# Kernel tuning notes

Measured on AMD Instinct MI355X. Metric: run time of the kernel, lower is better.

Reference implementation:

```python
import jax, jax.numpy as jnp
import numpy as np

N = 1024   # codeword length (variable nodes)
M_CN = 512 # check nodes
DV = 3     # variable-node degree
DC = 6     # check-node degree
E = N * DV # edges = 3072
B = 128    # batch of codewords
CLIP = 0.999999


def _build_masks():
    rng = np.random.default_rng(0)
    vn = np.repeat(np.arange(N), DV)                    # [E] variable node of each edge
    cn = rng.permutation(np.repeat(np.arange(M_CN), DC))  # [E] check node of each edge
    off = ~np.eye(E, dtype=bool)
    vn2cn = ((cn[:, None] == cn[None, :]) & off).astype(np.float32)  # [E,E] same check, excl self
    cn2vn = ((vn[:, None] == vn[None, :]) & off).astype(np.float32)  # [E,E] same vn, excl self
    onehot = (vn[:, None] == np.arange(N)[None, :]).astype(np.float32)  # [E,N]
    first = np.clip(vn2cn @ onehot, 0.0, 1.0)           # [E,N] vns in same check, excl own edge
    out_mask = onehot.T.copy()                          # [N,E]
    bias_mat = onehot.T.copy()                          # [N,E] routes LLR[v] to its edges
    return first, cn2vn, vn2cn, out_mask, bias_mat


def setup_inputs() -> dict:
    key = jax.random.key(0)
    x = jax.random.normal(key, (B, N), dtype=jnp.float32) * 2.0  # channel LLRs
    first, cn2vn, vn2cn, out_mask, bias_mat = _build_masks()
    return {
        "x": x,
        "first_mask": jnp.asarray(first),
        "cn2vn_mask": jnp.asarray(cn2vn),
        "vn2cn_mask": jnp.asarray(vn2cn),
        "out_mask": jnp.asarray(out_mask),
        "bias_mat": jnp.asarray(bias_mat),
    }


def _cn_update(x, mask):
    # Faithful to CnUpdateLayer: out[:,i] = prod_j of (x[:,j]*mask[i,j]) over nonzero
    # masked entries (masked-off or exactly-zero entries treated as 1), and 0 if no
    # nonzero masked entry. Computed fused in log/sign domain via matmuls instead of
    # the original per-column Python loop.
    nz = (x != 0.0)
    logabs = jnp.where(nz, jnp.log(jnp.abs(jnp.where(nz, x, 1.0))), 0.0)  # [B,I]
    neg = ((x < 0.0) & nz).astype(x.dtype)
    s = logabs @ mask.T                          # [B,O] sum log|x_j| over masked j
    negcnt = neg @ mask.T                        # [B,O] number of negative factors
    cnt = nz.astype(x.dtype) @ mask.T            # [B,O] number of nonzero factors
    sign = 1.0 - 2.0 * (negcnt % 2.0)
    return jnp.where(cnt > 0.0, sign * jnp.exp(s), 0.0)


def reference(x, first_mask, cn2vn_mask, vn2cn_mask, out_mask, bias_mat):
    llr = x  # Channel_LLR; bias_scaling_vectors are identity matrices (no-ops)
    bias = llr @ bias_mat  # [B,E], reused each iteration

    def cn_to_llr(h):
        return 2.0 * jnp.arctanh(jnp.clip(h, -CLIP, CLIP))

    h = jnp.tanh(0.5 * x)
    h = cn_to_llr(_cn_update(h, first_mask))          # fc0
    out1 = jax.nn.sigmoid(h @ out_mask.T + llr)

    h = jnp.tanh(0.5 * (h @ cn2vn_mask.T + bias))     # fc1
    h = cn_to_llr(_cn_update(h, vn2cn_mask))          # fc2
    out2 = jax.nn.sigmoid(h @ out_mask.T + llr)

    h = jnp.tanh(0.5 * (h @ cn2vn_mask.T + bias))     # fc3
    h = cn_to_llr(_cn_update(h, vn2cn_mask))          # fc4
    out3 = jax.nn.sigmoid(h @ out_mask.T + llr)

    h = jnp.tanh(0.5 * (h @ cn2vn_mask.T + bias))     # fc5
    h = cn_to_llr(_cn_update(h, vn2cn_mask))          # fc6
    out4 = jax.nn.sigmoid(h @ out_mask.T + llr)

    h = jnp.tanh(0.5 * (h @ cn2vn_mask.T + bias))     # fc7
    h = cn_to_llr(_cn_update(h, vn2cn_mask))          # fc8
    out5 = jax.nn.sigmoid(h @ out_mask.T + llr)       # fc9 (out_mask) + identity-scaled LLR

    return (out5, out4, out3, out2, out1)
```

## Files before the change

### kernel.cpp

```cpp
#include <hip/hip_runtime.h>
#include <math.h>

namespace {
constexpr int kN = 1024;
constexpr int kE = 3072;
constexpr int kB = 128;
constexpr float kClip = 0.999999f;
}

#define RCP(x) __builtin_amdgcn_rcpf(x)

__global__ __launch_bounds__(256) void extract_partners_kernel(
    const uint4* __restrict__ mask, unsigned long long* __restrict__ part) {
  __shared__ int slots[4][8];
  const int wave = threadIdx.x >> 6, lane = threadIdx.x & 63;
  const int row = blockIdx.x * 4 + wave;
  const uint4* rp = mask + (size_t)row * (kE / 4);
  const int it0 = (row + 1) >> 8;

  uint4 vals[12];
#pragma unroll
  for (int it = 0; it < 12; ++it)
    if (it >= it0) vals[it] = rp[it * 64 + lane];

  const unsigned long long lt = (1ULL << lane) - 1ULL;
  int cnt = 0;
#pragma unroll
  for (int it = 0; it < 12; ++it) {
    if (it < it0) continue;
    uint4 v = vals[it];
    const int idx = it * 256 + lane * 4;
    const bool b0 = (v.x != 0u) & (idx + 0 > row);
    const bool b1 = (v.y != 0u) & (idx + 1 > row);
    const bool b2 = (v.z != 0u) & (idx + 2 > row);
    const bool b3 = (v.w != 0u) & (idx + 3 > row);
    unsigned long long m0 = __ballot(b0);
    unsigned long long m1 = __ballot(b1);
    unsigned long long m2 = __ballot(b2);
    unsigned long long m3 = __ballot(b3);
    int before = cnt + __popcll(m0 & lt) + __popcll(m1 & lt) +
                 __popcll(m2 & lt) + __popcll(m3 & lt);
    int own = 0;
    if (b0) slots[wave][min(before + own, 7)] = idx + 0;
    own += (int)((m0 >> lane) & 1ULL);
    if (b1) slots[wave][min(before + own, 7)] = idx + 1;
    own += (int)((m1 >> lane) & 1ULL);
    if (b2) slots[wave][min(before + own, 7)] = idx + 2;
    own += (int)((m2 >> lane) & 1ULL);
    if (b3) slots[wave][min(before + own, 7)] = idx + 3;
    cnt += __popcll(m0) + __popcll(m1) + __popcll(m2) + __popcll(m3);
  }
  __syncthreads();
  if (cnt == 5 && lane < 6) {
    int g[6];
    g[0] = row;
#pragma unroll
    for (int i = 0; i < 5; ++i) g[i + 1] = slots[wave][i];
    unsigned long long pk = 0;
    int sh = 0;
#pragma unroll
    for (int i = 0; i < 6; ++i)
      if (i != lane) {
        pk |= (unsigned long long)(g[i] & 0xFFF) << sh;
        sh += 12;
      }
    part[g[lane]] = pk;
  }
}

__global__ __launch_bounds__(1024) void bp_kernel(
    const float* __restrict__ x, const unsigned long long* __restrict__ part,
    float* __restrict__ out) {
  __shared__ float tm[kE];
  __shared__ float rm[kE];
  const int b = blockIdx.x;
  const int tid = threadIdx.x;

  const unsigned long long pk0 = part[tid];
  const unsigned long long pk1 = part[tid + 1024];
  const unsigned long long pk2 = part[tid + 2048];
  const int i00 = (int)(pk0 & 0xFFF), i01 = (int)((pk0 >> 12) & 0xFFF),
            i02 = (int)((pk0 >> 24) & 0xFFF), i03 = (int)((pk0 >> 36) & 0xFFF),
            i04 = (int)((pk0 >> 48) & 0xFFF);
  const int i10 = (int)(pk1 & 0xFFF), i11 = (int)((pk1 >> 12) & 0xFFF),
            i12 = (int)((pk1 >> 24) & 0xFFF), i13 = (int)((pk1 >> 36) & 0xFFF),
            i14 = (int)((pk1 >> 48) & 0xFFF);
  const int i20 = (int)(pk2 & 0xFFF), i21 = (int)((pk2 >> 12) & 0xFFF),
            i22 = (int)((pk2 >> 24) & 0xFFF), i23 = (int)((pk2 >> 36) & 0xFFF),
            i24 = (int)((pk2 >> 48) & 0xFFF);

  const float l = x[(size_t)b * kN + tid];
  const float E = __expf(l);
  tm[tid] = (E - 1.0f) * RCP(E + 1.0f);
  __syncthreads();

  {
    const int ii[3][5] = {{i00, i01, i02, i03, i04},
                          {i10, i11, i12, i13, i14},
                          {i20, i21, i22, i23, i24}};
#pragma unroll
    for (int i = 0; i < 3; ++i) {
      const int q0 = ii[i][0] / 3, q1 = ii[i][1] / 3, q2 = ii[i][2] / 3,
                q3 = ii[i][3] / 3, q4 = ii[i][4] / 3;
      float prod = tm[q0];
      float f1 = tm[q1], f2 = tm[q2], f3 = tm[q3], f4 = tm[q4];
      prod *= (q1 == q0) ? 1.0f : f1;
      prod *= (q2 == q0 || q2 == q1) ? 1.0f : f2;
      prod *= (q3 == q0 || q3 == q1 || q3 == q2) ? 1.0f : f3;
      prod *= (q4 == q0 || q4 == q1 || q4 == q2 || q4 == q3) ? 1.0f : f4;
      const float y = fminf(fmaxf(prod, -kClip), kClip);
      rm[tid + i * 1024] = (1.0f + y) * RCP(1.0f - y);
    }
  }
  __syncthreads();

  float* ob = out + (size_t)b * kN + tid;
#pragma unroll
  for (int k = 1; k <= 4; ++k) {
    const float r0 = rm[3 * tid], r1 = rm[3 * tid + 1], r2 = rm[3 * tid + 2];
    const float P = E * r0 * r1 * r2;
    ob[(size_t)(5 - k) * kB * kN] = P * RCP(1.0f + P);
    const float p0 = E * r1 * r2, p1 = E * r0 * r2, p2 = E * r0 * r1;
    tm[3 * tid]     = (p0 - 1.0f) * RCP(p0 + 1.0f);
    tm[3 * tid + 1] = (p1 - 1.0f) * RCP(p1 + 1.0f);
    tm[3 * tid + 2] = (p2 - 1.0f) * RCP(p2 + 1.0f);
    __syncthreads();
    {
      float y0 = tm[i00] * tm[i01] * tm[i02] * tm[i03] * tm[i04];
      float y = fminf(fmaxf(y0, -kClip), kClip);
      rm[tid] = (1.0f + y) * RCP(1.0f - y);
      y0 = tm[i10] * tm[i11] * tm[i12] * tm[i13] * tm[i14];
      y = fminf(fmaxf(y0, -kClip), kClip);
      rm[tid + 1024] = (1.0f + y) * RCP(1.0f - y);
      y0 = tm[i20] * tm[i21] * tm[i22] * tm[i23] * tm[i24];
      y = fminf(fmaxf(y0, -kClip), kClip);
      rm[tid + 2048] = (1.0f + y) * RCP(1.0f - y);
    }
    __syncthreads();
  }
  const float r0 = rm[3 * tid], r1 = rm[3 * tid + 1], r2 = rm[3 * tid + 2];
  const float P = E * r0 * r1 * r2;
  ob[0] = P * RCP(1.0f + P);
}

extern "C" void kernel_launch(void* const* d_in, const int* in_sizes, int n_in,
                              void* d_out, int out_size, void* d_ws, size_t ws_size,
                              hipStream_t stream) {
  const float* x = (const float*)d_in[0];
  const float* vn2cn = (const float*)d_in[3];
  unsigned long long* part = (unsigned long long*)d_ws;
  float* out = (float*)d_out;

  hipLaunchKernelGGL(extract_partners_kernel, dim3(kE / 4), dim3(256), 0, stream,
                     (const uint4*)vn2cn, part);
  hipLaunchKernelGGL(bp_kernel, dim3(kB), dim3(1024), 0, stream, x, part, out);
}
```

Baseline: 18.90 us.

## Remap edges to threads so check results stay in registers, double-buffer shared messages

Each thread now owns the three edges of its own variable node for check-node updates, so check results stay in registers and the rm shared array plus its barrier go away. Shared messages are double-buffered so each iteration needs only one __syncthreads. The ratio products are rewritten as numerator/denominator pairs to drop some reciprocals. The partner loads become strided (part[3*tid+i]), which may reduce coalescing, and the ratio form may change rounding slightly.

```diff
diff --git a/kernel.cpp b/kernel.cpp
--- a/kernel.cpp
+++ b/kernel.cpp
@@ -71,76 +71,86 @@
 __global__ __launch_bounds__(1024) void bp_kernel(
     const float* __restrict__ x, const unsigned long long* __restrict__ part,
     float* __restrict__ out) {
-  __shared__ float tm[kE];
-  __shared__ float rm[kE];
+  __shared__ float tmV[kN];
+  __shared__ float tmE[2][kE];
   const int b = blockIdx.x;
   const int tid = threadIdx.x;
 
-  const unsigned long long pk0 = part[tid];
-  const unsigned long long pk1 = part[tid + 1024];
-  const unsigned long long pk2 = part[tid + 2048];
-  const int i00 = (int)(pk0 & 0xFFF), i01 = (int)((pk0 >> 12) & 0xFFF),
-            i02 = (int)((pk0 >> 24) & 0xFFF), i03 = (int)((pk0 >> 36) & 0xFFF),
-            i04 = (int)((pk0 >> 48) & 0xFFF);
-  const int i10 = (int)(pk1 & 0xFFF), i11 = (int)((pk1 >> 12) & 0xFFF),
-            i12 = (int)((pk1 >> 24) & 0xFFF), i13 = (int)((pk1 >> 36) & 0xFFF),
-            i14 = (int)((pk1 >> 48) & 0xFFF);
-  const int i20 = (int)(pk2 & 0xFFF), i21 = (int)((pk2 >> 12) & 0xFFF),
-            i22 = (int)((pk2 >> 24) & 0xFFF), i23 = (int)((pk2 >> 36) & 0xFFF),
-            i24 = (int)((pk2 >> 48) & 0xFFF);
+  int idx[3][5];
+#pragma unroll
+  for (int i = 0; i < 3; ++i) {
+    const unsigned long long pk = part[3 * tid + i];
+#pragma unroll
+    for (int j = 0; j < 5; ++j) idx[i][j] = (int)((pk >> (12 * j)) & 0xFFF);
+  }
 
   const float l = x[(size_t)b * kN + tid];
   const float E = __expf(l);
-  tm[tid] = (E - 1.0f) * RCP(E + 1.0f);
+  tmV[tid] = (E - 1.0f) * RCP(E + 1.0f);
   __syncthreads();
 
-  {
-    const int ii[3][5] = {{i00, i01, i02, i03, i04},
-                          {i10, i11, i12, i13, i14},
-                          {i20, i21, i22, i23, i24}};
+  float y[3];
 #pragma unroll
-    for (int i = 0; i < 3; ++i) {
-      const int q0 = ii[i][0] / 3, q1 = ii[i][1] / 3, q2 = ii[i][2] / 3,
-                q3 = ii[i][3] / 3, q4 = ii[i][4] / 3;
-      float prod = tm[q0];
-      float f1 = tm[q1], f2 = tm[q2], f3 = tm[q3], f4 = tm[q4];
-      prod *= (q1 == q0) ? 1.0f : f1;
-      prod *= (q2 == q0 || q2 == q1) ? 1.0f : f2;
-      prod *= (q3 == q0 || q3 == q1 || q3 == q2) ? 1.0f : f3;
-      prod *= (q4 == q0 || q4 == q1 || q4 == q2 || q4 == q3) ? 1.0f : f4;
-      const float y = fminf(fmaxf(prod, -kClip), kClip);
-      rm[tid + i * 1024] = (1.0f + y) * RCP(1.0f - y);
-    }
+  for (int i = 0; i < 3; ++i) {
+    const int q0 = idx[i][0] / 3, q1 = idx[i][1] / 3, q2 = idx[i][2] / 3,
+              q3 = idx[i][3] / 3, q4 = idx[i][4] / 3;
+    float prod = tmV[q0];
+    const float f1 = tmV[q1], f2 = tmV[q2], f3 = tmV[q3], f4 = tmV[q4];
+    prod *= (q1 == q0) ? 1.0f : f1;
+    prod *= (q2 == q0 || q2 == q1) ? 1.0f : f2;
+    prod *= (q3 == q0 || q3 == q1 || q3 == q2) ? 1.0f : f3;
+    prod *= (q4 == q0 || q4 == q1 || q4 == q2 || q4 == q3) ? 1.0f : f4;
+    y[i] = fminf(fmaxf(prod, -kClip), kClip);
   }
-  __syncthreads();
 
   float* ob = out + (size_t)b * kN + tid;
-#pragma unroll
-  for (int k = 1; k <= 4; ++k) {
-    const float r0 = rm[3 * tid], r1 = rm[3 * tid + 1], r2 = rm[3 * tid + 2];
-    const float P = E * r0 * r1 * r2;
-    ob[(size_t)(5 - k) * kB * kN] = P * RCP(1.0f + P);
-    const float p0 = E * r1 * r2, p1 = E * r0 * r2, p2 = E * r0 * r1;
-    tm[3 * tid]     = (p0 - 1.0f) * RCP(p0 + 1.0f);
-    tm[3 * tid + 1] = (p1 - 1.0f) * RCP(p1 + 1.0f);
-    tm[3 * tid + 2] = (p2 - 1.0f) * RCP(p2 + 1.0f);
-    __syncthreads();
-    {
-      float y0 = tm[i00] * tm[i01] * tm[i02] * tm[i03] * tm[i04];
-      float y = fminf(fmaxf(y0, -kClip), kClip);
-      rm[tid] = (1.0f + y) * RCP(1.0f - y);
-      y0 = tm[i10] * tm[i11] * tm[i12] * tm[i13] * tm[i14];
-      y = fminf(fmaxf(y0, -kClip), kClip);
-      rm[tid + 1024] = (1.0f + y) * RCP(1.0f - y);
-      y0 = tm[i20] * tm[i21] * tm[i22] * tm[i23] * tm[i24];
-      y = fminf(fmaxf(y0, -kClip), kClip);
-      rm[tid + 2048] = (1.0f + y) * RCP(1.0f - y);
-    }
-    __syncthreads();
+
+#define OUT_VN(slot, wbuf)                                                 \
+  {                                                                        \
+    const float a0 = 1.0f + y[0], a1 = 1.0f + y[1], a2 = 1.0f + y[2];      \
+    const float s0 = 1.0f - y[0], s1 = 1.0f - y[1], s2 = 1.0f - y[2];      \
+    const float Nn = E * a0 * a1 * a2;                                     \
+    const float Dd = s0 * s1 * s2;                                         \
+    ob[(size_t)(slot) * kB * kN] = Nn * RCP(Nn + Dd);                      \
+    const float n0 = E * a1 * a2, d0 = s1 * s2;                            \
+    const float n1 = E * a0 * a2, d1 = s0 * s2;                            \
+    const float n2 = E * a0 * a1, d2 = s0 * s1;                            \
+    (wbuf)[3 * tid + 0] = (n0 - d0) * RCP(n0 + d0);                        \
+    (wbuf)[3 * tid + 1] = (n1 - d1) * RCP(n1 + d1);                        \
+    (wbuf)[3 * tid + 2] = (n2 - d2) * RCP(n2 + d2);                        \
   }
-  const float r0 = rm[3 * tid], r1 = rm[3 * tid + 1], r2 = rm[3 * tid + 2];
-  const float P = E * r0 * r1 * r2;
-  ob[0] = P * RCP(1.0f + P);
+
+#define CN(rbuf)                                                           \
+  {                                                                        \
+    _Pragma("unroll") for (int i = 0; i < 3; ++i) {                        \
+      const float p = (rbuf)[idx[i][0]] * (rbuf)[idx[i][1]] *              \
+                      (rbuf)[idx[i][2]] * (rbuf)[idx[i][3]] *              \
+                      (rbuf)[idx[i][4]];                                   \
+      y[i] = fminf(fmaxf(p, -kClip), kClip);                               \
+    }                                                                      \
+  }
+
+  OUT_VN(4, tmE[0]);
+  __syncthreads();
+  CN(tmE[0]);
+  OUT_VN(3, tmE[1]);
+  __syncthreads();
+  CN(tmE[1]);
+  OUT_VN(2, tmE[0]);
+  __syncthreads();
+  CN(tmE[0]);
+  OUT_VN(1, tmE[1]);
+  __syncthreads();
+  CN(tmE[1]);
+  {
+    const float a0 = 1.0f + y[0], a1 = 1.0f + y[1], a2 = 1.0f + y[2];
+    const float s0 = 1.0f - y[0], s1 = 1.0f - y[1], s2 = 1.0f - y[2];
+    const float Nn = E * a0 * a1 * a2;
+    const float Dd = s0 * s1 * s2;
+    ob[0] = Nn * RCP(Nn + Dd);
+  }
+#undef OUT_VN
+#undef CN
 }
 
 extern "C" void kernel_launch(void* const* d_in, const int* in_sizes, int n_in,
```

Result: faster. 17.96 us, median of 2 (-4.9%).
